# Performance work log

Hardware: AMD Instinct MI355X
Metric: run time of the kernel (lower is better)

Reference implementation:

```python
import jax, jax.numpy as jnp
import numpy as np

NEG_INF = -9e15
ALPHA = 0.2  # LeakyReLU negative slope
OUT_FEATURES = 128


def setup_inputs() -> dict:
    key = jax.random.key(0)
    k1, k2, k3, k4 = jax.random.split(key, 4)
    B, N, F_in, F_out = 4, 4096, 256, OUT_FEATURES
    h = jax.random.normal(k1, (B, N, F_in), dtype=jnp.float32)
    adj = jax.random.randint(k2, (B, N, N), 0, 2, dtype=jnp.int32)
    W = jax.random.normal(k3, (F_in, F_out), dtype=jnp.float32) * 0.07
    a = jax.random.normal(k4, (2 * F_out, 1), dtype=jnp.float32) * 0.1
    return {"h": h, "adj": adj, "W": W, "a": a}


def reference(h, adj, W, a):
    # Wh: (B, N, F_out)
    Wh = jnp.einsum('bni,io->bno', h, W)
    a1 = a[:OUT_FEATURES, 0]   # (F_out,)
    a2 = a[OUT_FEATURES:, 0]   # (F_out,)
    Wh1 = Wh @ a1              # (B, N)
    Wh2 = Wh @ a2              # (B, N)
    e = Wh1[:, :, None] + Wh2[:, None, :]          # (B, N, N)
    e = jnp.where(e >= 0, e, ALPHA * e)             # LeakyReLU
    e = jnp.where(adj > 0, e, NEG_INF)              # adjacency mask
    attention = jax.nn.softmax(e, axis=-1)          # (B, N, N)
    # dropout omitted: reference runs in eval mode (training=False)
    h_prime = jnp.einsum('bnm,bmo->bno', attention, Wh)
    return jax.nn.elu(h_prime)  # concat=True
```

## Files before the change

kernel.cpp:

```cpp
#include <hip/hip_runtime.h>
#include <hip/hip_bf16.h>
#include <math.h>

typedef __attribute__((ext_vector_type(4))) float  f32x4;
typedef __attribute__((ext_vector_type(4))) int    i32x4;
typedef __attribute__((ext_vector_type(8))) short  s16x8;
typedef __attribute__((ext_vector_type(4))) short  s16x4;
typedef __attribute__((ext_vector_type(8))) __bf16 bf16x8;

#define LOG2E 1.4426950408889634f

__device__ __forceinline__ short f32_to_bf16_rne(float f) {
    unsigned u = __builtin_bit_cast(unsigned, f);
    u += 0x7fffu + ((u >> 16) & 1u);
    return (short)(u >> 16);
}
__device__ __forceinline__ int pack2_bf16(float f0, float f1) {
    unsigned u0 = __builtin_bit_cast(unsigned, f0) + 0x8000u;
    unsigned u1 = __builtin_bit_cast(unsigned, f1) + 0x8000u;
    return (int)((u0 >> 16) | (u1 & 0xffff0000u));
}
__device__ __forceinline__ bf16x8 as_bf16x8(s16x8 v) {
    return __builtin_bit_cast(bf16x8, v);
}
__device__ __forceinline__ bf16x8 as_bf16x8(i32x4 v) {
    return __builtin_bit_cast(bf16x8, v);
}

__global__ void k0_wt(const float* __restrict__ W, short* __restrict__ WT) {
    int g = blockIdx.x * 256 + threadIdx.x;
    int col = g >> 6;
    int k0 = (g & 63) * 4;
    s16x4 v;
    #pragma unroll
    for (int i = 0; i < 4; ++i) v[i] = f32_to_bf16_rne(W[(k0 + i) * 128 + col]);
    *(s16x4*)(WT + col * 256 + k0) = v;
}

__global__ __launch_bounds__(256, 2) void k1_gemm(
    const float* __restrict__ h, const float* __restrict__ a,
    const short* __restrict__ WT,
    short* __restrict__ WhT, float* __restrict__ Wh1p, float* __restrict__ Tp)
{
    int l = threadIdx.x & 63;
    int w = threadIdx.x >> 6;
    int gw = blockIdx.x * 4 + w;
    int r0 = gw * 16;
    int lm = l & 15, q = l >> 4;

    f32x4 acc[8];
    #pragma unroll
    for (int ct = 0; ct < 8; ++ct) acc[ct] = (f32x4)0.0f;

    const float* hrow = h + (long)(r0 + lm) * 256;
    for (int kb = 0; kb < 8; ++kb) {
        int kbase = kb * 32 + q * 8;
        f32x4 h0 = *(const f32x4*)(hrow + kbase);
        f32x4 h1 = *(const f32x4*)(hrow + kbase + 4);
        s16x8 af;
        #pragma unroll
        for (int j = 0; j < 4; ++j) af[j] = f32_to_bf16_rne(h0[j]);
        #pragma unroll
        for (int j = 0; j < 4; ++j) af[4 + j] = f32_to_bf16_rne(h1[j]);
        bf16x8 afb = as_bf16x8(af);
        #pragma unroll
        for (int ct = 0; ct < 8; ++ct) {
            s16x8 bf = *(const s16x8*)(WT + (ct * 16 + lm) * 256 + kbase);
            acc[ct] = __builtin_amdgcn_mfma_f32_16x16x32_bf16(afb, as_bf16x8(bf), acc[ct], 0, 0, 0);
        }
    }

    int b = r0 >> 12;
    int nb = r0 & 4095;
    float p1[4] = {0.f, 0.f, 0.f, 0.f}, p2[4] = {0.f, 0.f, 0.f, 0.f};
    #pragma unroll
    for (int ct = 0; ct < 8; ++ct) {
        int col = ct * 16 + lm;
        float a1c = a[col], a2c = a[128 + col];
        s16x4 vv;
        #pragma unroll
        for (int r = 0; r < 4; ++r) {
            float v = acc[ct][r];
            p1[r] += v * a1c;
            p2[r] += v * a2c;
            vv[r] = f32_to_bf16_rne(v);
        }
        *(s16x4*)(WhT + ((long)(b * 128 + col) * 4096 + nb + q * 4)) = vv;
    }
    #pragma unroll
    for (int off = 1; off < 16; off <<= 1) {
        #pragma unroll
        for (int r = 0; r < 4; ++r) {
            p1[r] += __shfl_xor(p1[r], off);
            p2[r] += __shfl_xor(p2[r], off);
        }
    }
    if (lm == 0) {
        #pragma unroll
        for (int r = 0; r < 4; ++r) {
            int row = r0 + q * 4 + r;
            Wh1p[row] = LOG2E * p1[r];
            Tp[row]   = LOG2E * p2[r];
        }
    }
}

__global__ void k2_tmax(const float* __restrict__ Tp, float* __restrict__ Tmax) {
    __shared__ float red[256];
    int b = blockIdx.x, t = threadIdx.x;
    float mx = -1e30f;
    for (int i = 0; i < 16; ++i) mx = fmaxf(mx, Tp[b * 4096 + t + i * 256]);
    red[t] = mx;
    __syncthreads();
    for (int s = 128; s > 0; s >>= 1) {
        if (t < s) red[t] = fmaxf(red[t], red[t + s]);
        __syncthreads();
    }
    if (t == 0) Tmax[b] = red[0];
}

template <int SPLIT>
__global__ __launch_bounds__(256, 4) void k3_attn(
    const int* __restrict__ adj, const short* __restrict__ WhT,
    const float* __restrict__ Wh1p, const float* __restrict__ Tp,
    const float* __restrict__ Tmax,
    float* __restrict__ U, float* __restrict__ Z)
{
    const int MSLICE = 4096 / SPLIT;
    const int MTILES = MSLICE / 64;
    __shared__ __align__(16) short tile[2][128 * 64];
    __shared__ __align__(16) float tps[4096 / SPLIT];

    int l = threadIdx.x & 63, w = threadIdx.x >> 6;
    int lm = l & 15, q = l >> 4;
    int bid = blockIdx.x;
    int p = bid & (4 * SPLIT - 1);
    int b  = p >> 2;
    int mh = p & (SPLIT - 1);
    int rg = bid / (4 * SPLIT);
    int n0 = rg * 64;
    int mbase = mh * MSLICE;

    int n_lane = n0 + w * 16 + lm;
    float sp = Wh1p[b * 4096 + n_lane];
    float xm = sp + Tmax[b];
    float Mrow = fmaxf(xm, 0.2f * xm);

    const int*   adjrow = adj + ((long)(b * 4096 + n_lane) << 12) + q * 8;
    const short* whtb   = WhT + (long)b * 128 * 4096;
    const float* tpsq   = tps + q * 8;

    {
        const float* tg = Tp + b * 4096 + mbase;
        int i0 = threadIdx.x * 4;
        *(f32x4*)(tps + i0) = *(const f32x4*)(tg + i0);
    }

    f32x4 acc[8];
    #pragma unroll
    for (int ct = 0; ct < 8; ++ct) acc[ct] = (f32x4)0.0f;
    float z = 0.0f;

    auto stage = [&](short* dst, int m0) {
        int colw = w * 32;
        #pragma unroll
        for (int j = 0; j < 4; ++j) {
            int cb = colw + j * 8;
            int col = cb + (l >> 3);
            int gch = (l & 7) ^ (col & 7);
            const short* gp = whtb + (long)col * 4096 + m0 + gch * 8;
            __builtin_amdgcn_global_load_lds(
                (const __attribute__((address_space(1))) void*)gp,
                (__attribute__((address_space(3))) void*)(dst + cb * 64), 16, 0, 0);
        }
    };
    auto ldadj = [&](i32x4* aj, int m0) {
        #pragma unroll
        for (int ks = 0; ks < 2; ++ks) {
            aj[2 * ks]     = *(const i32x4*)(adjrow + m0 + ks * 32);
            aj[2 * ks + 1] = *(const i32x4*)(adjrow + m0 + ks * 32 + 4);
        }
    };
    auto compute = [&](const short* buf, const i32x4* aj, int mrel) {
        #pragma unroll
        for (int ks = 0; ks < 2; ++ks) {
            f32x4 t0 = *(const f32x4*)(tpsq + mrel + ks * 32);
            f32x4 t1 = *(const f32x4*)(tpsq + mrel + ks * 32 + 4);
            i32x4 pk;
            float zs = 0.0f;
            #pragma unroll
            for (int half = 0; half < 2; ++half) {
                i32x4 a4 = aj[2 * ks + half];
                f32x4 t4 = half ? t1 : t0;
                float wv[4];
                #pragma unroll
                for (int j = 0; j < 4; ++j) {
                    float y = sp + t4[j];
                    float e = fmaxf(y, 0.2f * y) - Mrow;
                    float v = __builtin_amdgcn_exp2f(e);
                    v = (a4[j] != 0) ? v : 0.0f;
                    zs += v; wv[j] = v;
                }
                pk[half * 2]     = pack2_bf16(wv[0], wv[1]);
                pk[half * 2 + 1] = pack2_bf16(wv[2], wv[3]);
            }
            z += zs;
            bf16x8 ab = as_bf16x8(pk);
            #pragma unroll
            for (int ct = 0; ct < 8; ++ct) {
                int col = ct * 16 + lm;
                int pos = (ks * 4 + q) ^ (col & 7);
                s16x8 bf = *(const s16x8*)(buf + col * 64 + pos * 8);
                acc[ct] = __builtin_amdgcn_mfma_f32_16x16x32_bf16(ab, as_bf16x8(bf), acc[ct], 0, 0, 0);
            }
        }
    };

    i32x4 ajA[4], ajB[4];
    stage(tile[0], mbase);
    ldadj(ajA, mbase);
    __syncthreads();

    #pragma unroll 1
    for (int t = 0; t < MTILES; t += 2) {
        int r1 = (t + 1) & (MTILES - 1);
        stage(tile[1], mbase + r1 * 64);
        ldadj(ajB, mbase + r1 * 64);
        __builtin_amdgcn_sched_barrier(0);
        compute(tile[0], ajA, t * 64);
        __syncthreads();
        int r2 = (t + 2) & (MTILES - 1);
        stage(tile[0], mbase + r2 * 64);
        ldadj(ajA, mbase + r2 * 64);
        __builtin_amdgcn_sched_barrier(0);
        compute(tile[1], ajB, r1 * 64);
        __syncthreads();
    }

    z += __shfl_xor(z, 16);
    z += __shfl_xor(z, 32);

    int slice = b * SPLIT + mh;
    if (l < 16) Z[slice * 4096 + n0 + w * 16 + lm] = z;
    float* ub = U + ((long)slice * 4096 + n0 + w * 16) * 128;
    #pragma unroll
    for (int ct = 0; ct < 8; ++ct) {
        int col = ct * 16 + lm;
        #pragma unroll
        for (int r = 0; r < 4; ++r)
            ub[(q * 4 + r) * 128 + col] = acc[ct][r];
    }
}

__global__ void k4_combine(const float* __restrict__ U, const float* __restrict__ Z,
                           float* __restrict__ out) {
    const long S = (long)4096 * 128;
    long g = (long)blockIdx.x * 256 + threadIdx.x;
    long off = g * 4;
    long nf = off >> 7;
    int b = (int)(nf >> 12), n = (int)(nf & 4095), col = (int)(off & 127);
    long base0 = ((long)(b * 4) * 4096 + n) * 128 + col;
    f32x4 u0 = *(const f32x4*)(U + base0);
    f32x4 u1 = *(const f32x4*)(U + base0 + S);
    f32x4 u2 = *(const f32x4*)(U + base0 + 2 * S);
    f32x4 u3 = *(const f32x4*)(U + base0 + 3 * S);
    float zz = Z[(b * 4 + 0) * 4096 + n] + Z[(b * 4 + 1) * 4096 + n]
             + Z[(b * 4 + 2) * 4096 + n] + Z[(b * 4 + 3) * 4096 + n];
    f32x4 v;
    #pragma unroll
    for (int i = 0; i < 4; ++i) {
        float x = (u0[i] + u1[i] + u2[i] + u3[i]) / zz;
        v[i] = (x > 0.f) ? x : (expf(x) - 1.0f);
    }
    *(f32x4*)(out + off) = v;
}

extern "C" void kernel_launch(void* const* d_in, const int* in_sizes, int n_in,
                              void* d_out, int out_size, void* d_ws, size_t ws_size,
                              hipStream_t stream) {
    const float* h   = (const float*)d_in[0];
    const int*   adj = (const int*)d_in[1];
    const float* W   = (const float*)d_in[2];
    const float* a   = (const float*)d_in[3];
    float* out = (float*)d_out;

    char* ws = (char*)d_ws;
    short* WhT  = (short*)ws;
    short* WT   = (short*)(ws + 4194304);
    float* Wh1p = (float*)(ws + 4259840);
    float* Tp   = (float*)(ws + 4325376);
    float* Tmax = (float*)(ws + 4390912);
    float* U    = (float*)(ws + 4391168);
    float* Z    = (float*)(ws + 4391168 + 33554432);

    k0_wt<<<32, 256, 0, stream>>>(W, WT);
    k1_gemm<<<256, 256, 0, stream>>>(h, a, WT, WhT, Wh1p, Tp);
    k2_tmax<<<4, 256, 0, stream>>>(Tp, Tmax);
    k3_attn<4><<<1024, 256, 0, stream>>>(adj, WhT, Wh1p, Tp, Tmax, U, Z);
    k4_combine<<<2048, 256, 0, stream>>>(U, Z, out);
    (void)in_sizes; (void)n_in; (void)out_size; (void)ws_size;
}
```

Baseline: 465.3 us.

## Load Wh B-fragments directly from global into registers instead of LDS tiles

Removes the LDS double-buffered staging of the WhT tile and instead has each lane load its MFMA B operands straight from global memory into registers, with adjacency loads prefetched four steps ahead. This drops the per-tile __syncthreads barriers and LDS traffic. It also fixes the batch index to p / SPLIT. In exchange, each of the four waves fetches the same WhT data separately from global/L2, and the B loads for the next step are issued only right after the current compute, so latency hiding is shallow.

```diff
diff --git a/kernel.cpp b/kernel.cpp
--- a/kernel.cpp
+++ b/kernel.cpp
@@ -127,15 +127,15 @@
     float* __restrict__ U, float* __restrict__ Z)
 {
     const int MSLICE = 4096 / SPLIT;
-    const int MTILES = MSLICE / 64;
-    __shared__ __align__(16) short tile[2][128 * 64];
+    const int MITERS = MSLICE / 32;
+    const int MM = MSLICE - 1;
     __shared__ __align__(16) float tps[4096 / SPLIT];
 
     int l = threadIdx.x & 63, w = threadIdx.x >> 6;
     int lm = l & 15, q = l >> 4;
     int bid = blockIdx.x;
     int p = bid & (4 * SPLIT - 1);
-    int b  = p >> 2;
+    int b  = p / SPLIT;
     int mh = p & (SPLIT - 1);
     int rg = bid / (4 * SPLIT);
     int n0 = rg * 64;
@@ -147,7 +147,7 @@
     float Mrow = fmaxf(xm, 0.2f * xm);
 
     const int*   adjrow = adj + ((long)(b * 4096 + n_lane) << 12) + q * 8;
-    const short* whtb   = WhT + (long)b * 128 * 4096;
+    const short* wcol   = WhT + (long)b * 128 * 4096 + (long)lm * 4096 + q * 8;
     const float* tpsq   = tps + q * 8;
 
     {
@@ -155,86 +155,73 @@
         int i0 = threadIdx.x * 4;
         *(f32x4*)(tps + i0) = *(const f32x4*)(tg + i0);
     }
+    __syncthreads();
 
     f32x4 acc[8];
     #pragma unroll
     for (int ct = 0; ct < 8; ++ct) acc[ct] = (f32x4)0.0f;
     float z = 0.0f;
 
-    auto stage = [&](short* dst, int m0) {
-        int colw = w * 32;
-        #pragma unroll
-        for (int j = 0; j < 4; ++j) {
-            int cb = colw + j * 8;
-            int col = cb + (l >> 3);
-            int gch = (l & 7) ^ (col & 7);
-            const short* gp = whtb + (long)col * 4096 + m0 + gch * 8;
-            __builtin_amdgcn_global_load_lds(
-                (const __attribute__((address_space(1))) void*)gp,
-                (__attribute__((address_space(3))) void*)(dst + cb * 64), 16, 0, 0);
-        }
+    auto ldB = [&](s16x8* Bf, int m) {
+        #pragma unroll
+        for (int ct = 0; ct < 8; ++ct)
+            Bf[ct] = *(const s16x8*)(wcol + (long)ct * 65536 + m);
     };
-    auto ldadj = [&](i32x4* aj, int m0) {
-        #pragma unroll
-        for (int ks = 0; ks < 2; ++ks) {
-            aj[2 * ks]     = *(const i32x4*)(adjrow + m0 + ks * 32);
-            aj[2 * ks + 1] = *(const i32x4*)(adjrow + m0 + ks * 32 + 4);
-        }
+    auto ldA = [&](i32x4* av, int m) {
+        av[0] = *(const i32x4*)(adjrow + m);
+        av[1] = *(const i32x4*)(adjrow + m + 4);
     };
-    auto compute = [&](const short* buf, const i32x4* aj, int mrel) {
-        #pragma unroll
-        for (int ks = 0; ks < 2; ++ks) {
-            f32x4 t0 = *(const f32x4*)(tpsq + mrel + ks * 32);
-            f32x4 t1 = *(const f32x4*)(tpsq + mrel + ks * 32 + 4);
-            i32x4 pk;
-            float zs = 0.0f;
+    auto compute = [&](const s16x8* Bf, const i32x4* av, int mrel) {
+        f32x4 t0 = *(const f32x4*)(tpsq + mrel);
+        f32x4 t1 = *(const f32x4*)(tpsq + mrel + 4);
+        i32x4 pk;
+        float zs = 0.0f;
+        #pragma unroll
+        for (int half = 0; half < 2; ++half) {
+            i32x4 a4 = av[half];
+            f32x4 t4 = half ? t1 : t0;
+            float wv[4];
             #pragma unroll
-            for (int half = 0; half < 2; ++half) {
-                i32x4 a4 = aj[2 * ks + half];
-                f32x4 t4 = half ? t1 : t0;
-                float wv[4];
-                #pragma unroll
-                for (int j = 0; j < 4; ++j) {
-                    float y = sp + t4[j];
-                    float e = fmaxf(y, 0.2f * y) - Mrow;
-                    float v = __builtin_amdgcn_exp2f(e);
-                    v = (a4[j] != 0) ? v : 0.0f;
-                    zs += v; wv[j] = v;
-                }
-                pk[half * 2]     = pack2_bf16(wv[0], wv[1]);
-                pk[half * 2 + 1] = pack2_bf16(wv[2], wv[3]);
+            for (int j = 0; j < 4; ++j) {
+                float y = sp + t4[j];
+                float e = fmaxf(y, 0.2f * y) - Mrow;
+                float v = __builtin_amdgcn_exp2f(e);
+                v = (a4[j] != 0) ? v : 0.0f;
+                zs += v; wv[j] = v;
             }
-            z += zs;
-            bf16x8 ab = as_bf16x8(pk);
-            #pragma unroll
-            for (int ct = 0; ct < 8; ++ct) {
-                int col = ct * 16 + lm;
-                int pos = (ks * 4 + q) ^ (col & 7);
-                s16x8 bf = *(const s16x8*)(buf + col * 64 + pos * 8);
-                acc[ct] = __builtin_amdgcn_mfma_f32_16x16x32_bf16(ab, as_bf16x8(bf), acc[ct], 0, 0, 0);
-            }
-        }
+            pk[half * 2]     = pack2_bf16(wv[0], wv[1]);
+            pk[half * 2 + 1] = pack2_bf16(wv[2], wv[3]);
+        }
+        z += zs;
+        bf16x8 ab = as_bf16x8(pk);
+        #pragma unroll
+        for (int ct = 0; ct < 8; ++ct)
+            acc[ct] = __builtin_amdgcn_mfma_f32_16x16x32_bf16(ab, as_bf16x8(Bf[ct]), acc[ct], 0, 0, 0);
     };
 
-    i32x4 ajA[4], ajB[4];
-    stage(tile[0], mbase);
-    ldadj(ajA, mbase);
-    __syncthreads();
+    s16x8 Ba[8];
+    i32x4 av0[2], av1[2], av2[2], av3[2];
+    ldB(Ba, mbase);
+    ldA(av0, mbase);
+    ldA(av1, mbase + 32);
+    ldA(av2, mbase + 64);
+    ldA(av3, mbase + 96);
 
     #pragma unroll 1
-    for (int t = 0; t < MTILES; t += 2) {
-        int r1 = (t + 1) & (MTILES - 1);
-        stage(tile[1], mbase + r1 * 64);
-        ldadj(ajB, mbase + r1 * 64);
-        __builtin_amdgcn_sched_barrier(0);
-        compute(tile[0], ajA, t * 64);
-        __syncthreads();
-        int r2 = (t + 2) & (MTILES - 1);
-        stage(tile[0], mbase + r2 * 64);
-        ldadj(ajA, mbase + r2 * 64);
-        __builtin_amdgcn_sched_barrier(0);
-        compute(tile[1], ajB, r1 * 64);
-        __syncthreads();
+    for (int i = 0; i < MITERS; i += 4) {
+        int mr = i * 32;
+        compute(Ba, av0, mr);
+        ldB(Ba, mbase + ((mr + 32) & MM));
+        ldA(av0, mbase + ((mr + 128) & MM));
+        compute(Ba, av1, mr + 32);
+        ldB(Ba, mbase + ((mr + 64) & MM));
+        ldA(av1, mbase + ((mr + 160) & MM));
+        compute(Ba, av2, mr + 64);
+        ldB(Ba, mbase + ((mr + 96) & MM));
+        ldA(av2, mbase + ((mr + 192) & MM));
+        compute(Ba, av3, mr + 96);
+        ldB(Ba, mbase + ((mr + 128) & MM));
+        ldA(av3, mbase + ((mr + 224) & MM));
     }
 
     z += __shfl_xor(z, 16);
```

Result: slower. 506.4 us (+8.8%).

## Prepack adjacency into LDS bitmask and widen WhT tiles to 128 columns

Applied to the files above, without the earlier changes.

The kernel now reads each block's adjacency slice up front with coalesced row-wise loads and compresses it into a swizzled 1-bit-per-entry bitmask in shared memory. It no longer streams int32 adjacency per lane inside the main loop. The WhT staging tile is doubled to 128 m-columns per step, halving the loop iterations and barriers, and launch bounds drop to 2 waves per SIMD to fit the larger LDS footprint. The batch index formula changes from p>>2 to p/SPLIT. The cost is a serialized adjacency prologue and lower occupancy, which may expose global-load latency in the main loop.

```diff
diff --git a/kernel.cpp b/kernel.cpp
--- a/kernel.cpp
+++ b/kernel.cpp
@@ -120,35 +120,62 @@
 }
 
 template <int SPLIT>
-__global__ __launch_bounds__(256, 4) void k3_attn(
+__global__ __launch_bounds__(256, 2) void k3_attn(
     const int* __restrict__ adj, const short* __restrict__ WhT,
     const float* __restrict__ Wh1p, const float* __restrict__ Tp,
     const float* __restrict__ Tmax,
     float* __restrict__ U, float* __restrict__ Z)
 {
     const int MSLICE = 4096 / SPLIT;
-    const int MTILES = MSLICE / 64;
-    __shared__ __align__(16) short tile[2][128 * 64];
+    const int MTILES = MSLICE / 128;
+    __shared__ __align__(16) short tile[2][128 * 128];
     __shared__ __align__(16) float tps[4096 / SPLIT];
+    __shared__ unsigned bm[64][32];
 
     int l = threadIdx.x & 63, w = threadIdx.x >> 6;
     int lm = l & 15, q = l >> 4;
     int bid = blockIdx.x;
     int p = bid & (4 * SPLIT - 1);
-    int b  = p >> 2;
+    int b  = p / SPLIT;
     int mh = p & (SPLIT - 1);
     int rg = bid / (4 * SPLIT);
     int n0 = rg * 64;
     int mbase = mh * MSLICE;
 
     int n_lane = n0 + w * 16 + lm;
+    int rrow = w * 16 + lm;
     float sp = Wh1p[b * 4096 + n_lane];
     float xm = sp + Tmax[b];
     float Mrow = fmaxf(xm, 0.2f * xm);
 
-    const int*   adjrow = adj + ((long)(b * 4096 + n_lane) << 12) + q * 8;
-    const short* whtb   = WhT + (long)b * 128 * 4096;
-    const float* tpsq   = tps + q * 8;
+    const short* whtb = WhT + (long)b * 128 * 4096;
+    const float* tpsq = tps + q * 8;
+
+    {
+        const int* base = adj + ((long)(b * 4096 + n0 + w * 16) << 12) + mbase;
+        unsigned short* bmh = (unsigned short*)bm;
+        #pragma unroll 1
+        for (int g = 0; g < 4; ++g) {
+            i32x4 v[4][4];
+            #pragma unroll
+            for (int rr = 0; rr < 4; ++rr) {
+                const int* rp = base + ((long)(g * 4 + rr) << 12) + l * 4;
+                #pragma unroll
+                for (int c = 0; c < 4; ++c) v[rr][c] = *(const i32x4*)(rp + c * 256);
+            }
+            #pragma unroll
+            for (int rr = 0; rr < 4; ++rr) {
+                unsigned bitsv = 0;
+                #pragma unroll
+                for (int c = 0; c < 4; ++c)
+                    #pragma unroll
+                    for (int j = 0; j < 4; ++j)
+                        bitsv |= (v[rr][c][j] != 0) ? (1u << (c * 4 + j)) : 0u;
+                int r = w * 16 + g * 4 + rr;
+                bmh[r * 64 + (((l >> 1) ^ (r & 31)) << 1) + (l & 1)] = (unsigned short)bitsv;
+            }
+        }
+    }
 
     {
         const float* tg = Tp + b * 4096 + mbase;
@@ -164,33 +191,29 @@
     auto stage = [&](short* dst, int m0) {
         int colw = w * 32;
         #pragma unroll
-        for (int j = 0; j < 4; ++j) {
-            int cb = colw + j * 8;
-            int col = cb + (l >> 3);
-            int gch = (l & 7) ^ (col & 7);
+        for (int j = 0; j < 8; ++j) {
+            int cb = colw + j * 4;
+            int col = cb + q;
+            int gch = lm ^ (col & 7);
             const short* gp = whtb + (long)col * 4096 + m0 + gch * 8;
             __builtin_amdgcn_global_load_lds(
                 (const __attribute__((address_space(1))) void*)gp,
-                (__attribute__((address_space(3))) void*)(dst + cb * 64), 16, 0, 0);
+                (__attribute__((address_space(3))) void*)(dst + cb * 128), 16, 0, 0);
         }
     };
-    auto ldadj = [&](i32x4* aj, int m0) {
-        #pragma unroll
-        for (int ks = 0; ks < 2; ++ks) {
-            aj[2 * ks]     = *(const i32x4*)(adjrow + m0 + ks * 32);
-            aj[2 * ks + 1] = *(const i32x4*)(adjrow + m0 + ks * 32 + 4);
-        }
-    };
-    auto compute = [&](const short* buf, const i32x4* aj, int mrel) {
-        #pragma unroll
-        for (int ks = 0; ks < 2; ++ks) {
+    auto compute = [&](const short* buf, int trel) {
+        int mrel = trel * 128;
+        int shiftc = (trel >> 1) * 4;
+        #pragma unroll
+        for (int ks = 0; ks < 4; ++ks) {
+            unsigned rd = bm[rrow][((16 * trel + 4 * ks + q) & 31) ^ (rrow & 31)];
+            unsigned mask8 = ((rd >> shiftc) & 0xFu) | (((rd >> (16 + shiftc)) & 0xFu) << 4);
             f32x4 t0 = *(const f32x4*)(tpsq + mrel + ks * 32);
             f32x4 t1 = *(const f32x4*)(tpsq + mrel + ks * 32 + 4);
             i32x4 pk;
             float zs = 0.0f;
             #pragma unroll
             for (int half = 0; half < 2; ++half) {
-                i32x4 a4 = aj[2 * ks + half];
                 f32x4 t4 = half ? t1 : t0;
                 float wv[4];
                 #pragma unroll
@@ -198,7 +221,7 @@
                     float y = sp + t4[j];
                     float e = fmaxf(y, 0.2f * y) - Mrow;
                     float v = __builtin_amdgcn_exp2f(e);
-                    v = (a4[j] != 0) ? v : 0.0f;
+                    v = (mask8 & (1u << (half * 4 + j))) ? v : 0.0f;
                     zs += v; wv[j] = v;
                 }
                 pk[half * 2]     = pack2_bf16(wv[0], wv[1]);
@@ -210,30 +233,24 @@
             for (int ct = 0; ct < 8; ++ct) {
                 int col = ct * 16 + lm;
                 int pos = (ks * 4 + q) ^ (col & 7);
-                s16x8 bf = *(const s16x8*)(buf + col * 64 + pos * 8);
+                s16x8 bf = *(const s16x8*)(buf + col * 128 + pos * 8);
                 acc[ct] = __builtin_amdgcn_mfma_f32_16x16x32_bf16(ab, as_bf16x8(bf), acc[ct], 0, 0, 0);
             }
         }
     };
 
-    i32x4 ajA[4], ajB[4];
     stage(tile[0], mbase);
-    ldadj(ajA, mbase);
     __syncthreads();
 
     #pragma unroll 1
     for (int t = 0; t < MTILES; t += 2) {
-        int r1 = (t + 1) & (MTILES - 1);
-        stage(tile[1], mbase + r1 * 64);
-        ldadj(ajB, mbase + r1 * 64);
+        stage(tile[1], mbase + ((t + 1) & (MTILES - 1)) * 128);
         __builtin_amdgcn_sched_barrier(0);
-        compute(tile[0], ajA, t * 64);
+        compute(tile[0], t);
         __syncthreads();
-        int r2 = (t + 2) & (MTILES - 1);
-        stage(tile[0], mbase + r2 * 64);
-        ldadj(ajA, mbase + r2 * 64);
+        stage(tile[0], mbase + ((t + 2) & (MTILES - 1)) * 128);
         __builtin_amdgcn_sched_barrier(0);
-        compute(tile[1], ajB, r1 * 64);
+        compute(tile[1], t + 1);
         __syncthreads();
     }
 
```

Result: faster. 440.2 us (-5.4%).
